# Performance work log

Hardware: AMD Instinct MI355X
Metric: run time of the kernel (lower is better)

The kernel has to match this reference:

```python
import jax, jax.numpy as jnp
import numpy as np

N, E, G = 20000, 320000, 16
IN, HID, OUT, HEADS = 256, 64, 256, 4
D0 = HID * HEADS  # 256, output dim of layer 0 (concat)


def _p(key, shape, scale=0.05):
    return (jax.random.normal(key, shape, dtype=jnp.float32) * scale)


def setup_inputs() -> dict:
    key = jax.random.key(0)
    ks = jax.random.split(key, 24)
    x = jax.random.normal(ks[0], (N, IN), dtype=jnp.float32)
    edge_index = jax.random.randint(ks[1], (2, E), 0, N, dtype=jnp.int64)
    batch = jnp.sort(jax.random.randint(ks[2], (N,), 0, G, dtype=jnp.int64))
    d = {"x": x, "edge_index": edge_index, "batch": batch}
    # Layer 0: TransformerConv(256 -> 64, heads=4, concat=True, beta=True)
    d["Wq0"] = _p(ks[3], (IN, D0)); d["bq0"] = jnp.zeros((D0,), jnp.float32)
    d["Wk0"] = _p(ks[4], (IN, D0)); d["bk0"] = jnp.zeros((D0,), jnp.float32)
    d["Wv0"] = _p(ks[5], (IN, D0)); d["bv0"] = jnp.zeros((D0,), jnp.float32)
    d["Ws0"] = _p(ks[6], (IN, D0)); d["bs0"] = jnp.zeros((D0,), jnp.float32)
    d["Wb0"] = _p(ks[7], (3 * D0, 1))
    d["g0"] = jnp.ones((D0,), jnp.float32); d["b0"] = jnp.zeros((D0,), jnp.float32)
    # Layer 1: TransformerConv(256 -> 256, heads=1, concat=False, beta=True)
    d["Wq1"] = _p(ks[8], (D0, OUT)); d["bq1"] = jnp.zeros((OUT,), jnp.float32)
    d["Wk1"] = _p(ks[9], (D0, OUT)); d["bk1"] = jnp.zeros((OUT,), jnp.float32)
    d["Wv1"] = _p(ks[10], (D0, OUT)); d["bv1"] = jnp.zeros((OUT,), jnp.float32)
    d["Ws1"] = _p(ks[11], (D0, OUT)); d["bs1"] = jnp.zeros((OUT,), jnp.float32)
    d["Wb1"] = _p(ks[12], (3 * OUT, 1))
    d["g1"] = jnp.ones((OUT,), jnp.float32); d["b1"] = jnp.zeros((OUT,), jnp.float32)
    return d


def _transformer_conv(x, src, dst, Wq, bq, Wk, bk, Wv, bv, Ws, bs, Wb, H, C, concat):
    n = x.shape[0]
    q = (x @ Wq + bq).reshape(n, H, C)
    k = (x @ Wk + bk).reshape(n, H, C)
    v = (x @ Wv + bv).reshape(n, H, C)
    # per-edge attention logits [E, H]
    alpha = (q[dst] * k[src]).sum(-1) / jnp.sqrt(jnp.asarray(C, jnp.float32))
    # segment softmax over incoming edges of each dst node
    m = jax.ops.segment_max(alpha, dst, num_segments=n)  # [N, H]
    a = jnp.exp(alpha - m[dst])
    s = jax.ops.segment_sum(a, dst, num_segments=n)  # [N, H]
    a = a / s[dst]
    out = jax.ops.segment_sum(a[:, :, None] * v[src], dst, num_segments=n)  # [N,H,C]
    out = out.reshape(n, H * C) if concat else out.mean(axis=1)
    # beta-gated skip connection
    r = x @ Ws + bs
    g = jax.nn.sigmoid(jnp.concatenate([out, r, out - r], axis=-1) @ Wb)  # [N,1]
    return g * r + (1.0 - g) * out


def _layer_norm(x, g, b, eps=1e-5):
    mu = x.mean(-1, keepdims=True)
    var = x.var(-1, keepdims=True)
    return (x - mu) * jax.lax.rsqrt(var + eps) * g + b


def reference(x, edge_index, batch,
              Wq0, bq0, Wk0, bk0, Wv0, bv0, Ws0, bs0, Wb0, g0, b0,
              Wq1, bq1, Wk1, bk1, Wv1, bv1, Ws1, bs1, Wb1, g1, b1):
    src, dst = edge_index[0], edge_index[1]
    h = _transformer_conv(x, src, dst, Wq0, bq0, Wk0, bk0, Wv0, bv0, Ws0, bs0, Wb0, HEADS, HID, True)
    h = jax.nn.relu(_layer_norm(h, g0, b0))  # dropout is identity at inference
    h = _transformer_conv(h, src, dst, Wq1, bq1, Wk1, bk1, Wv1, bv1, Ws1, bs1, Wb1, 1, OUT, False)
    h = _layer_norm(h, g1, b1)
    # global mean pool over graphs
    sums = jax.ops.segment_sum(h, batch, num_segments=G)
    counts = jax.ops.segment_sum(jnp.ones((h.shape[0],), h.dtype), batch, num_segments=G)
    return sums / jnp.maximum(counts, 1.0)[:, None]
```

## Files before the change

kernel.cpp:

```cpp
#include <hip/hip_runtime.h>
#include <hip/hip_bf16.h>


#define DEVFN static __device__ __forceinline__

typedef __attribute__((ext_vector_type(4))) float f32x4;
typedef __attribute__((ext_vector_type(2))) float f32x2;
typedef __attribute__((ext_vector_type(8))) short bf16x8;

DEVFN float bfu2f(unsigned short u) {
    union { unsigned int i; float f; } t; t.i = ((unsigned)u) << 16; return t.f;
}
DEVFN unsigned short f2bu(float f) {
    __hip_bfloat16 b = __float2bfloat16(f);
    return __builtin_bit_cast(unsigned short, b);
}
DEVFN void stb4(__hip_bfloat16* p, float4 v) {
    ushort4 u;
    u.x = f2bu(v.x); u.y = f2bu(v.y); u.z = f2bu(v.z); u.w = f2bu(v.w);
    *reinterpret_cast<ushort4*>(p) = u;
}
DEVFN float4 f8x4_to_f4(unsigned u) {
    const f32x2 lo = __builtin_amdgcn_cvt_pk_f32_fp8((int)u, false);
    const f32x2 hi = __builtin_amdgcn_cvt_pk_f32_fp8((int)u, true);
    return make_float4(lo.x, lo.y, hi.x, hi.y);
}

DEVFN float dot16(const float* q, uint4 u) {
    const float4 f0 = f8x4_to_f4(u.x);
    const float4 f1 = f8x4_to_f4(u.y);
    const float4 f2 = f8x4_to_f4(u.z);
    const float4 f3 = f8x4_to_f4(u.w);
    float p;
    p = q[0] * f0.x;            p = fmaf(q[1],  f0.y, p);
    p = fmaf(q[2],  f0.z, p);   p = fmaf(q[3],  f0.w, p);
    p = fmaf(q[4],  f1.x, p);   p = fmaf(q[5],  f1.y, p);
    p = fmaf(q[6],  f1.z, p);   p = fmaf(q[7],  f1.w, p);
    p = fmaf(q[8],  f2.x, p);   p = fmaf(q[9],  f2.y, p);
    p = fmaf(q[10], f2.z, p);   p = fmaf(q[11], f2.w, p);
    p = fmaf(q[12], f3.x, p);   p = fmaf(q[13], f3.y, p);
    p = fmaf(q[14], f3.z, p);   p = fmaf(q[15], f3.w, p);
    return p;
}
DEVFN void accum16(float* acc, uint4 u, float a) {
    const float4 f0 = f8x4_to_f4(u.x);
    const float4 f1 = f8x4_to_f4(u.y);
    const float4 f2 = f8x4_to_f4(u.z);
    const float4 f3 = f8x4_to_f4(u.w);
    acc[0]  = fmaf(a, f0.x, acc[0]);  acc[1]  = fmaf(a, f0.y, acc[1]);
    acc[2]  = fmaf(a, f0.z, acc[2]);  acc[3]  = fmaf(a, f0.w, acc[3]);
    acc[4]  = fmaf(a, f1.x, acc[4]);  acc[5]  = fmaf(a, f1.y, acc[5]);
    acc[6]  = fmaf(a, f1.z, acc[6]);  acc[7]  = fmaf(a, f1.w, acc[7]);
    acc[8]  = fmaf(a, f2.x, acc[8]);  acc[9]  = fmaf(a, f2.y, acc[9]);
    acc[10] = fmaf(a, f2.z, acc[10]); acc[11] = fmaf(a, f2.w, acc[11]);
    acc[12] = fmaf(a, f3.x, acc[12]); acc[13] = fmaf(a, f3.y, acc[13]);
    acc[14] = fmaf(a, f3.z, acc[14]); acc[15] = fmaf(a, f3.w, acc[15]);
}

__global__ __launch_bounds__(256)
void wconv_kernel(const float* __restrict__ W0, const float* __restrict__ W1,
                  const float* __restrict__ W2, const float* __restrict__ W3,
                  const float* __restrict__ W4, const float* __restrict__ W5,
                  const float* __restrict__ W6, const float* __restrict__ W7,
                  __hip_bfloat16* __restrict__ Wt)
{
    const float* W;
    switch (blockIdx.y) {
        case 0: W = W0; break; case 1: W = W1; break;
        case 2: W = W2; break; case 3: W = W3; break;
        case 4: W = W4; break; case 5: W = W5; break;
        case 6: W = W6; break; default: W = W7; break;
    }
    const int k = blockIdx.x;
    const int c = threadIdx.x;
    Wt[(size_t)blockIdx.y * 65536 + (size_t)c * 256 + k] =
        __float2bfloat16(W[(size_t)k * 256 + c]);
}

#define SWZ64(r, kb) ((r) * 128 + ((kb) ^ (((r) & 7) << 4)))
#define TSTRIDE 272

template <bool AF32>
__global__ __launch_bounds__(256)
void gemm_mfma_kernel(const void* __restrict__ Av, int M,
                      const __hip_bfloat16* __restrict__ Wt,
                      const float* __restrict__ b0, const float* __restrict__ b1,
                      const float* __restrict__ b2, const float* __restrict__ b3,
                      void* __restrict__ O0, void* __restrict__ O1,
                      void* __restrict__ O2, void* __restrict__ O3,
                      int s0, int s1, int s2, int s3,
                      int f0, int f1, int f2, int f3)
{
    const int q8   = gridDim.x >> 3;
    const int wgid = (blockIdx.x & 7) * q8 + (blockIdx.x >> 3);
    const int rowblk = wgid >> 3;
    const int rem    = wgid & 7;
    const int colblk = rem >> 2;
    const int z      = rem & 3;

    const float* bias; void* O; int rs, isf8;
    switch (z) {
        case 0:  bias = b0; O = O0; rs = s0; isf8 = f0; break;
        case 1:  bias = b1; O = O1; rs = s1; isf8 = f1; break;
        case 2:  bias = b2; O = O2; rs = s2; isf8 = f2; break;
        default: bias = b3; O = O3; rs = s3; isf8 = f3; break;
    }
    const __hip_bfloat16* Wz = Wt + (size_t)z * 65536;

    __shared__ __align__(16) char Sh[128 * TSTRIDE];
    char* As = Sh;
    char* Bs = Sh + 16384;

    const int tid  = threadIdx.x;
    const int row0 = rowblk * 128;
    const int col0 = colblk * 128;
    const int wid  = tid >> 6, lane = tid & 63;
    const int wr   = wid >> 1, wc = wid & 1;
    const int lrow = lane & 15, kg = lane >> 4;

    const int chunk = tid & 7;
    const int rsub  = tid >> 3;

    f32x4 acc[4][4] = {};

    for (int k0 = 0; k0 < 256; k0 += 64) {
        #pragma unroll
        for (int p = 0; p < 4; ++p) {
            const int r  = p * 32 + rsub;
            const int gr = row0 + r;

            if (AF32) {
                const float* Af = (const float*)Av;
                ushort4 lo = {0, 0, 0, 0}, hi = {0, 0, 0, 0};
                if (gr < M) {
                    const float4 a = *reinterpret_cast<const float4*>(
                        Af + (size_t)gr * 256 + k0 + chunk * 8);
                    const float4 b = *reinterpret_cast<const float4*>(
                        Af + (size_t)gr * 256 + k0 + chunk * 8 + 4);
                    lo.x = f2bu(a.x); lo.y = f2bu(a.y); lo.z = f2bu(a.z); lo.w = f2bu(a.w);
                    hi.x = f2bu(b.x); hi.y = f2bu(b.y); hi.z = f2bu(b.z); hi.w = f2bu(b.w);
                }
                *reinterpret_cast<ushort4*>(As + SWZ64(r, chunk * 16))     = lo;
                *reinterpret_cast<ushort4*>(As + SWZ64(r, chunk * 16) + 8) = hi;
            } else {
                const __hip_bfloat16* Ab = (const __hip_bfloat16*)Av;
                ulonglong2 av = {0ull, 0ull};
                if (gr < M)
                    av = *reinterpret_cast<const ulonglong2*>(
                        Ab + (size_t)gr * 256 + k0 + chunk * 8);
                *reinterpret_cast<ulonglong2*>(As + SWZ64(r, chunk * 16)) = av;
            }

            const ulonglong2 bv = *reinterpret_cast<const ulonglong2*>(
                Wz + (size_t)(col0 + r) * 256 + k0 + chunk * 8);
            *reinterpret_cast<ulonglong2*>(Bs + SWZ64(r, chunk * 16)) = bv;
        }
        __syncthreads();

        #pragma unroll
        for (int kk = 0; kk < 64; kk += 32) {
            const int kbyte = kk * 2 + kg * 16;
            bf16x8 af[4], bfr[4];
            #pragma unroll
            for (int m = 0; m < 4; ++m) {
                const int r = wr * 64 + m * 16 + lrow;
                af[m] = *reinterpret_cast<const bf16x8*>(As + SWZ64(r, kbyte));
            }
            #pragma unroll
            for (int n = 0; n < 4; ++n) {
                const int c = wc * 64 + n * 16 + lrow;
                bfr[n] = *reinterpret_cast<const bf16x8*>(Bs + SWZ64(c, kbyte));
            }
            #pragma unroll
            for (int m = 0; m < 4; ++m)
                #pragma unroll
                for (int n = 0; n < 4; ++n)
                    acc[m][n] = __builtin_amdgcn_mfma_f32_16x16x32_bf16(
                        af[m], bfr[n], acc[m][n], 0, 0, 0);
        }
        __syncthreads();
    }

    #pragma unroll
    for (int m = 0; m < 4; ++m) {
        #pragma unroll
        for (int j = 0; j < 4; ++j) {
            const int rr = wr * 64 + m * 16 + kg * 4 + j;
            #pragma unroll
            for (int n = 0; n < 4; ++n) {
                const int cc = wc * 64 + n * 16 + lrow;
                const float v = acc[m][n][j] + bias[col0 + cc];
                *reinterpret_cast<unsigned short*>(Sh + rr * TSTRIDE + cc * 2) = f2bu(v);
            }
        }
    }
    __syncthreads();

    const int row  = tid >> 1;
    const int half = tid & 1;
    const int grow = row0 + row;
    if (grow >= M) return;
    const char* src = Sh + row * TSTRIDE + half * 128;

    if (isf8) {
        unsigned char* dst = (unsigned char*)O + (size_t)grow * rs + col0 + half * 64;
        #pragma unroll
        for (int i2 = 0; i2 < 4; ++i2) {
            uint4 w;
            unsigned tmp[4];
            #pragma unroll
            for (int c8 = 0; c8 < 2; ++c8) {
                const bf16x8 e = *reinterpret_cast<const bf16x8*>(src + (i2 * 2 + c8) * 16);
                const int p0 = __builtin_amdgcn_cvt_pk_fp8_f32(
                    bfu2f((unsigned short)e[0]), bfu2f((unsigned short)e[1]), 0, false);
                const int p1 = __builtin_amdgcn_cvt_pk_fp8_f32(
                    bfu2f((unsigned short)e[2]), bfu2f((unsigned short)e[3]), 0, false);
                const int p2 = __builtin_amdgcn_cvt_pk_fp8_f32(
                    bfu2f((unsigned short)e[4]), bfu2f((unsigned short)e[5]), 0, false);
                const int p3 = __builtin_amdgcn_cvt_pk_fp8_f32(
                    bfu2f((unsigned short)e[6]), bfu2f((unsigned short)e[7]), 0, false);
                tmp[c8 * 2 + 0] = (unsigned)(p0 & 0xFFFF) | ((unsigned)(p1 & 0xFFFF) << 16);
                tmp[c8 * 2 + 1] = (unsigned)(p2 & 0xFFFF) | ((unsigned)(p3 & 0xFFFF) << 16);
            }
            w.x = tmp[0]; w.y = tmp[1]; w.z = tmp[2]; w.w = tmp[3];
            *reinterpret_cast<uint4*>(dst + i2 * 16) = w;
        }
    } else {
        char* dst = (char*)((__hip_bfloat16*)O + (size_t)grow * rs + col0 + half * 64);
        #pragma unroll
        for (int i = 0; i < 8; ++i)
            *reinterpret_cast<ulonglong2*>(dst + i * 16) =
                *reinterpret_cast<const ulonglong2*>(src + i * 16);
    }
}

__global__ __launch_bounds__(256)
void build_kernel(const int* __restrict__ ei, int E, int* __restrict__ deg, int nhist,
                  const int* __restrict__ batch, int N, int* __restrict__ gcount)
{
    if (blockIdx.x < nhist) {
        const int e = blockIdx.x * 256 + threadIdx.x;
        if (e < E) atomicAdd(&deg[ei[E + e]], 1);
    } else {
        __shared__ int h[16];
        if (threadIdx.x < 16) h[threadIdx.x] = 0;
        __syncthreads();
        const int n = (blockIdx.x - nhist) * 256 + threadIdx.x;
        if (n < N) atomicAdd(&h[batch[n]], 1);
        __syncthreads();
        if (threadIdx.x < 16 && h[threadIdx.x] != 0)
            atomicAdd(&gcount[threadIdx.x], h[threadIdx.x]);
    }
}

__global__ __launch_bounds__(1024)
void scan_kernel(const int* __restrict__ deg, int* __restrict__ row_start, int n,
                 const int* __restrict__ gcount, int* __restrict__ gstart)
{
    __shared__ int wsum[16];
    __shared__ int wincl[16];
    const int tid  = threadIdx.x;
    const int w    = tid >> 6;
    const int lane = tid & 63;
    if (tid == 0) {
        row_start[0] = 0;
        int o = 0;
        #pragma unroll
        for (int g = 0; g < 16; ++g) { gstart[g] = o; o += gcount[g]; }
        gstart[16] = o;
    }
    int offset = 0;
    for (int base = 0; base < n; base += 1024) {
        const int idx = base + tid;
        int s = (idx < n) ? deg[idx] : 0;
        #pragma unroll
        for (int d = 1; d < 64; d <<= 1) {
            const int t = __shfl_up(s, d, 64);
            if (lane >= d) s += t;
        }
        if (lane == 63) wsum[w] = s;
        __syncthreads();
        if (tid < 16) {
            int si = wsum[tid];
            #pragma unroll
            for (int d = 1; d < 16; d <<= 1) {
                const int u = __shfl_up(si, d, 64);
                if (tid >= d) si += u;
            }
            wincl[tid] = si;
        }
        __syncthreads();
        const int woff = (w > 0) ? wincl[w - 1] : 0;
        if (idx < n) row_start[idx + 1] = offset + woff + s;
        offset += wincl[15];
        __syncthreads();
    }
}

__global__ __launch_bounds__(256)
void fill_kernel(const int* __restrict__ ei, int E,
                 const int* __restrict__ row_start,
                 int* __restrict__ cursor, int* __restrict__ csr_src)
{
    const int e = blockIdx.x * 256 + threadIdx.x;
    if (e >= E) return;
    const int s = ei[e];
    const int d = ei[E + e];
    const int pos = atomicAdd(&cursor[d], 1);
    csr_src[row_start[d] + pos] = s;
}

template <int NSH, bool RELU, bool OUTB>
__global__ __launch_bounds__(128)
void attn_kernel(const __hip_bfloat16* __restrict__ Q,
                 const unsigned char* __restrict__ KV,
                 const __hip_bfloat16* __restrict__ R,
                 const float* __restrict__ Wb, const float* __restrict__ lng,
                 const float* __restrict__ lnb,
                 const int* __restrict__ row_start, const int* __restrict__ csr_src,
                 __hip_bfloat16* __restrict__ outb, float* __restrict__ outf,
                 int N, float scale)
{
    const int wv   = threadIdx.x >> 6;
    const int lane = threadIdx.x & 63;
    const int g    = lane >> 4;
    const int s    = lane & 15;
    const int node = blockIdx.x * 2 + wv;
    if (node >= N) return;

    float q[16];
    {
        const bf16x8 a = *reinterpret_cast<const bf16x8*>(Q + (size_t)node * 256 + s * 16);
        const bf16x8 b = *reinterpret_cast<const bf16x8*>(Q + (size_t)node * 256 + s * 16 + 8);
        #pragma unroll
        for (int j = 0; j < 8; ++j) {
            q[j]     = bfu2f((unsigned short)a[j]);
            q[8 + j] = bfu2f((unsigned short)b[j]);
        }
    }

    const int beg = row_start[node];
    const int end = row_start[node + 1];

    float acc[16] = {};
    float ssum = 0.f;

    int i = beg + g;
    for (; i + 4 < end; i += 8) {
        const int sa = csr_src[i];
        const int sb = csr_src[i + 4];
        const uint4 ka = *reinterpret_cast<const uint4*>(KV + (size_t)sa * 512 + s * 16);
        const uint4 va = *reinterpret_cast<const uint4*>(KV + (size_t)sa * 512 + 256 + s * 16);
        const uint4 kb = *reinterpret_cast<const uint4*>(KV + (size_t)sb * 512 + s * 16);
        const uint4 vb = *reinterpret_cast<const uint4*>(KV + (size_t)sb * 512 + 256 + s * 16);
        float pa = dot16(q, ka);
        float pb = dot16(q, kb);
        #pragma unroll
        for (int m = 1; m < (1 << NSH); m <<= 1) {
            pa += __shfl_xor(pa, m, 64);
            pb += __shfl_xor(pb, m, 64);
        }
        const float aa = __expf(pa * scale);
        const float ab = __expf(pb * scale);
        ssum += aa + ab;
        accum16(acc, va, aa);
        accum16(acc, vb, ab);
    }
    if (i < end) {
        const int sa = csr_src[i];
        const uint4 ka = *reinterpret_cast<const uint4*>(KV + (size_t)sa * 512 + s * 16);
        const uint4 va = *reinterpret_cast<const uint4*>(KV + (size_t)sa * 512 + 256 + s * 16);
        float pa = dot16(q, ka);
        #pragma unroll
        for (int m = 1; m < (1 << NSH); m <<= 1) pa += __shfl_xor(pa, m, 64);
        const float aa = __expf(pa * scale);
        ssum += aa;
        accum16(acc, va, aa);
    }

    ssum += __shfl_xor(ssum, 16, 64);
    ssum += __shfl_xor(ssum, 32, 64);
    #pragma unroll
    for (int j = 0; j < 16; ++j) {
        acc[j] += __shfl_xor(acc[j], 16, 64);
        acc[j] += __shfl_xor(acc[j], 32, 64);
    }

    if (g != 0) return;

    const float is = (ssum > 0.f) ? 1.f / ssum : 0.f;
    float o[16];
    #pragma unroll
    for (int j = 0; j < 16; ++j) o[j] = acc[j] * is;

    float r[16];
    {
        const bf16x8 a = *reinterpret_cast<const bf16x8*>(R + (size_t)node * 256 + s * 16);
        const bf16x8 b = *reinterpret_cast<const bf16x8*>(R + (size_t)node * 256 + s * 16 + 8);
        #pragma unroll
        for (int j = 0; j < 8; ++j) {
            r[j]     = bfu2f((unsigned short)a[j]);
            r[8 + j] = bfu2f((unsigned short)b[j]);
        }
    }

    float z = 0.f;
    #pragma unroll
    for (int j = 0; j < 16; ++j) {
        const int d = s * 16 + j;
        z += o[j] * Wb[d] + r[j] * Wb[256 + d] + (o[j] - r[j]) * Wb[512 + d];
    }
    #pragma unroll
    for (int m = 1; m < 16; m <<= 1) z += __shfl_xor(z, m, 64);
    const float gg = 1.f / (1.f + __expf(-z));

    float h[16];
    float s1 = 0.f, s2 = 0.f;
    #pragma unroll
    for (int j = 0; j < 16; ++j) {
        h[j] = gg * r[j] + (1.f - gg) * o[j];
        s1 += h[j];
        s2 += h[j] * h[j];
    }
    #pragma unroll
    for (int m = 1; m < 16; m <<= 1) {
        s1 += __shfl_xor(s1, m, 64);
        s2 += __shfl_xor(s2, m, 64);
    }
    const float mu  = s1 * (1.f / 256.f);
    const float var = s2 * (1.f / 256.f) - mu * mu;
    const float inv = rsqrtf(var + 1e-5f);

    #pragma unroll
    for (int j = 0; j < 16; ++j) {
        const int d = s * 16 + j;
        h[j] = (h[j] - mu) * inv * lng[d] + lnb[d];
        if (RELU) h[j] = fmaxf(h[j], 0.f);
    }

    if (OUTB) {
        __hip_bfloat16* dst = outb + (size_t)node * 256 + s * 16;
        stb4(dst,      make_float4(h[0],  h[1],  h[2],  h[3]));
        stb4(dst + 4,  make_float4(h[4],  h[5],  h[6],  h[7]));
        stb4(dst + 8,  make_float4(h[8],  h[9],  h[10], h[11]));
        stb4(dst + 12, make_float4(h[12], h[13], h[14], h[15]));
    } else {
        float* dst = outf + (size_t)node * 256 + s * 16;
        #pragma unroll
        for (int c4 = 0; c4 < 4; ++c4)
            *reinterpret_cast<float4*>(dst + c4 * 4) =
                make_float4(h[c4 * 4], h[c4 * 4 + 1], h[c4 * 4 + 2], h[c4 * 4 + 3]);
    }
}

__global__ __launch_bounds__(256)
void pool_partial_kernel(const float* __restrict__ h, const int* __restrict__ gstart,
                         float* __restrict__ partial)
{
    const int s    = blockIdx.x;
    const int g    = blockIdx.y;
    const int tid  = threadIdx.x;
    const int quad = tid & 63;
    const int sub  = tid >> 6;

    const int beg = gstart[g];
    const int cnt = gstart[g + 1] - beg;

    f32x4 acc = {0.f, 0.f, 0.f, 0.f};
    for (int i = s * 4 + sub; i < cnt; i += 64) {
        const f32x4 v = *reinterpret_cast<const f32x4*>(
            h + (size_t)(beg + i) * 256 + quad * 4);
        acc += v;
    }

    __shared__ f32x4 sh[4][64];
    sh[sub][quad] = acc;
    __syncthreads();
    if (sub == 0) {
        const f32x4 r = sh[0][quad] + sh[1][quad] + sh[2][quad] + sh[3][quad];
        *reinterpret_cast<f32x4*>(partial + ((size_t)(g * 16 + s) * 64 + quad) * 4) = r;
    }
}

__global__ __launch_bounds__(256)
void pool_final_kernel(const float* __restrict__ partial, const int* __restrict__ gcount,
                       float* __restrict__ out)
{
    const int g = blockIdx.x;
    const int d = threadIdx.x;
    float sum = 0.f;
    #pragma unroll
    for (int s = 0; s < 16; ++s)
        sum += partial[(size_t)(g * 16 + s) * 256 + d];
    out[(size_t)g * 256 + d] = sum / (float)max(gcount[g], 1);
}

extern "C" void kernel_launch(void* const* d_in, const int* in_sizes, int n_in,
                              void* d_out, int out_size, void* d_ws, size_t ws_size,
                              hipStream_t stream)
{
    const float* x     = (const float*)d_in[0];
    const int*   ei    = (const int*)d_in[1];
    const int*   batch = (const int*)d_in[2];
    const float* Wq0 = (const float*)d_in[3];  const float* bq0 = (const float*)d_in[4];
    const float* Wk0 = (const float*)d_in[5];  const float* bk0 = (const float*)d_in[6];
    const float* Wv0 = (const float*)d_in[7];  const float* bv0 = (const float*)d_in[8];
    const float* Ws0 = (const float*)d_in[9];  const float* bs0 = (const float*)d_in[10];
    const float* Wb0 = (const float*)d_in[11];
    const float* g0  = (const float*)d_in[12]; const float* b0  = (const float*)d_in[13];
    const float* Wq1 = (const float*)d_in[14]; const float* bq1 = (const float*)d_in[15];
    const float* Wk1 = (const float*)d_in[16]; const float* bk1 = (const float*)d_in[17];
    const float* Wv1 = (const float*)d_in[18]; const float* bv1 = (const float*)d_in[19];
    const float* Ws1 = (const float*)d_in[20]; const float* bs1 = (const float*)d_in[21];
    const float* Wb1 = (const float*)d_in[22];
    const float* g1  = (const float*)d_in[23]; const float* b1  = (const float*)d_in[24];

    const int N = in_sizes[0] / 256;
    const int E = in_sizes[1] / 2;
    const int G = 16;
    const size_t NM = (size_t)N * 256;

    __hip_bfloat16* bws = (__hip_bfloat16*)d_ws;
    __hip_bfloat16* qb  = bws;
    __hip_bfloat16* rb  = qb  + NM;
    __hip_bfloat16* h0b = rb  + NM;
    __hip_bfloat16* wt  = h0b + NM;
    unsigned char* kvb  = (unsigned char*)(wt + 8 * 65536);
    float* h1f     = (float*)(kvb + (size_t)N * 512);
    float* partial = h1f + NM;
    int* deg       = (int*)(partial + 16 * 16 * 256);
    int* row_start = deg + N;
    int* cursor    = row_start + N + 1;
    int* gcount    = cursor + N;
    int* gstart    = gcount + G;
    int* csr_src   = gstart + 17;

    const size_t zbytes = ((size_t)N + (N + 1) + N + G + 17) * sizeof(int);
    hipMemsetAsync(deg, 0, zbytes, stream);

    const int eb = (E + 255) / 256;
    const int nb = (N + 255) / 256;

    wconv_kernel<<<dim3(256, 8), 256, 0, stream>>>(Wq0, Wk0, Wv0, Ws0,
                                                   Wq1, Wk1, Wv1, Ws1, wt);

    build_kernel<<<eb + nb, 256, 0, stream>>>(ei, E, deg, eb, batch, N, gcount);
    scan_kernel<<<1, 1024, 0, stream>>>(deg, row_start, N, gcount, gstart);
    fill_kernel<<<eb, 256, 0, stream>>>(ei, E, row_start, cursor, csr_src);

    const int nrb   = (N + 127) / 128;
    const int ggrid = nrb * 8;
    const int agrid = (N + 1) / 2;

    gemm_mfma_kernel<true><<<ggrid, 256, 0, stream>>>(x, N, wt,
        bq0, bk0, bv0, bs0,
        qb, kvb, kvb + 256, rb,
        256, 512, 512, 256,
        0, 1, 1, 0);
    attn_kernel<2, true, true><<<agrid, 128, 0, stream>>>(
        qb, kvb, rb, Wb0, g0, b0, row_start, csr_src, h0b, nullptr, N, 0.125f);

    gemm_mfma_kernel<false><<<ggrid, 256, 0, stream>>>(h0b, N, wt + 4 * 65536,
        bq1, bk1, bv1, bs1,
        qb, kvb, kvb + 256, rb,
        256, 512, 512, 256,
        0, 1, 1, 0);
    attn_kernel<4, false, false><<<agrid, 128, 0, stream>>>(
        qb, kvb, rb, Wb1, g1, b1, row_start, csr_src, nullptr, h1f, N, 0.0625f);

    pool_partial_kernel<<<dim3(16, 16), 256, 0, stream>>>(h1f, gstart, partial);
    pool_final_kernel<<<16, 256, 0, stream>>>(partial, gcount, (float*)d_out);
}
```

Measured before the change: 232.0 us.

## Pre-convert x to bf16 and stage GEMM tiles with direct global-to-LDS loads

```diff
diff --git a/kernel.cpp b/kernel.cpp
--- a/kernel.cpp
+++ b/kernel.cpp
@@ -7,6 +7,10 @@
 typedef __attribute__((ext_vector_type(4))) float f32x4;
 typedef __attribute__((ext_vector_type(2))) float f32x2;
 typedef __attribute__((ext_vector_type(8))) short bf16x8;
+
+#define GLOAD16(g, lds) __builtin_amdgcn_global_load_lds(                      \
+    (const __attribute__((address_space(1))) unsigned int*)(g),                \
+    (__attribute__((address_space(3))) unsigned int*)(lds), 16, 0, 0)
 
 DEVFN float bfu2f(unsigned short u) {
     union { unsigned int i; float f; } t; t.i = ((unsigned)u) << 16; return t.f;
@@ -58,31 +62,40 @@
 }
 
 __global__ __launch_bounds__(256)
-void wconv_kernel(const float* __restrict__ W0, const float* __restrict__ W1,
-                  const float* __restrict__ W2, const float* __restrict__ W3,
-                  const float* __restrict__ W4, const float* __restrict__ W5,
-                  const float* __restrict__ W6, const float* __restrict__ W7,
-                  __hip_bfloat16* __restrict__ Wt)
-{
-    const float* W;
-    switch (blockIdx.y) {
-        case 0: W = W0; break; case 1: W = W1; break;
-        case 2: W = W2; break; case 3: W = W3; break;
-        case 4: W = W4; break; case 5: W = W5; break;
-        case 6: W = W6; break; default: W = W7; break;
-    }
-    const int k = blockIdx.x;
-    const int c = threadIdx.x;
-    Wt[(size_t)blockIdx.y * 65536 + (size_t)c * 256 + k] =
-        __float2bfloat16(W[(size_t)k * 256 + c]);
+void prep_kernel(const float* __restrict__ x, __hip_bfloat16* __restrict__ xb, int nf2b,
+                 const float* __restrict__ W0, const float* __restrict__ W1,
+                 const float* __restrict__ W2, const float* __restrict__ W3,
+                 const float* __restrict__ W4, const float* __restrict__ W5,
+                 const float* __restrict__ W6, const float* __restrict__ W7,
+                 __hip_bfloat16* __restrict__ Wt)
+{
+    const int b = blockIdx.x;
+    if (b < nf2b) {
+        const int i = b * 256 + threadIdx.x;
+        const float4 v = *reinterpret_cast<const float4*>(x + (size_t)i * 4);
+        stb4(xb + (size_t)i * 4, v);
+    } else {
+        const int wb = b - nf2b;
+        const int z  = wb >> 8;
+        const int k  = wb & 255;
+        const int c  = threadIdx.x;
+        const float* W;
+        switch (z) {
+            case 0: W = W0; break; case 1: W = W1; break;
+            case 2: W = W2; break; case 3: W = W3; break;
+            case 4: W = W4; break; case 5: W = W5; break;
+            case 6: W = W6; break; default: W = W7; break;
+        }
+        Wt[(size_t)z * 65536 + (size_t)c * 256 + k] =
+            __float2bfloat16(W[(size_t)k * 256 + c]);
+    }
 }
 
 #define SWZ64(r, kb) ((r) * 128 + ((kb) ^ (((r) & 7) << 4)))
 #define TSTRIDE 272
 
-template <bool AF32>
 __global__ __launch_bounds__(256)
-void gemm_mfma_kernel(const void* __restrict__ Av, int M,
+void gemm_mfma_kernel(const __hip_bfloat16* __restrict__ A, int M,
                       const __hip_bfloat16* __restrict__ Wt,
                       const float* __restrict__ b0, const float* __restrict__ b1,
                       const float* __restrict__ b2, const float* __restrict__ b3,
@@ -118,42 +131,21 @@
     const int wr   = wid >> 1, wc = wid & 1;
     const int lrow = lane & 15, kg = lane >> 4;
 
-    const int chunk = tid & 7;
-    const int rsub  = tid >> 3;
-
     f32x4 acc[4][4] = {};
 
     for (int k0 = 0; k0 < 256; k0 += 64) {
         #pragma unroll
-        for (int p = 0; p < 4; ++p) {
-            const int r  = p * 32 + rsub;
+        for (int j = 0; j < 4; ++j) {
+            const int s_lin = j * 4096 + wid * 1024 + lane * 16;
+            const int r     = s_lin >> 7;
+            const int kb    = (s_lin & 127) ^ ((r & 7) << 4);
+            const int kelem = k0 + (kb >> 1);
+            char* ldsA = As + j * 4096 + wid * 1024;
+            char* ldsB = Bs + j * 4096 + wid * 1024;
             const int gr = row0 + r;
-
-            if (AF32) {
-                const float* Af = (const float*)Av;
-                ushort4 lo = {0, 0, 0, 0}, hi = {0, 0, 0, 0};
-                if (gr < M) {
-                    const float4 a = *reinterpret_cast<const float4*>(
-                        Af + (size_t)gr * 256 + k0 + chunk * 8);
-                    const float4 b = *reinterpret_cast<const float4*>(
-                        Af + (size_t)gr * 256 + k0 + chunk * 8 + 4);
-                    lo.x = f2bu(a.x); lo.y = f2bu(a.y); lo.z = f2bu(a.z); lo.w = f2bu(a.w);
-                    hi.x = f2bu(b.x); hi.y = f2bu(b.y); hi.z = f2bu(b.z); hi.w = f2bu(b.w);
-                }
-                *reinterpret_cast<ushort4*>(As + SWZ64(r, chunk * 16))     = lo;
-                *reinterpret_cast<ushort4*>(As + SWZ64(r, chunk * 16) + 8) = hi;
-            } else {
-                const __hip_bfloat16* Ab = (const __hip_bfloat16*)Av;
-                ulonglong2 av = {0ull, 0ull};
-                if (gr < M)
-                    av = *reinterpret_cast<const ulonglong2*>(
-                        Ab + (size_t)gr * 256 + k0 + chunk * 8);
-                *reinterpret_cast<ulonglong2*>(As + SWZ64(r, chunk * 16)) = av;
-            }
-
-            const ulonglong2 bv = *reinterpret_cast<const ulonglong2*>(
-                Wz + (size_t)(col0 + r) * 256 + k0 + chunk * 8);
-            *reinterpret_cast<ulonglong2*>(Bs + SWZ64(r, chunk * 16)) = bv;
+            if (gr < M)
+                GLOAD16(A + (size_t)gr * 256 + kelem, ldsA);
+            GLOAD16(Wz + (size_t)(col0 + r) * 256 + kelem, ldsB);
         }
         __syncthreads();
 
@@ -521,7 +513,8 @@
     const size_t NM = (size_t)N * 256;
 
     __hip_bfloat16* bws = (__hip_bfloat16*)d_ws;
-    __hip_bfloat16* qb  = bws;
+    __hip_bfloat16* xb  = bws;
+    __hip_bfloat16* qb  = xb  + NM;
     __hip_bfloat16* rb  = qb  + NM;
     __hip_bfloat16* h0b = rb  + NM;
     __hip_bfloat16* wt  = h0b + NM;
@@ -540,9 +533,10 @@
 
     const int eb = (E + 255) / 256;
     const int nb = (N + 255) / 256;
-
-    wconv_kernel<<<dim3(256, 8), 256, 0, stream>>>(Wq0, Wk0, Wv0, Ws0,
-                                                   Wq1, Wk1, Wv1, Ws1, wt);
+    const int nf2b = (int)((NM / 4 + 255) / 256);
+
+    prep_kernel<<<nf2b + 2048, 256, 0, stream>>>(x, xb, nf2b,
+        Wq0, Wk0, Wv0, Ws0, Wq1, Wk1, Wv1, Ws1, wt);
 
     build_kernel<<<eb + nb, 256, 0, stream>>>(ei, E, deg, eb, batch, N, gcount);
     scan_kernel<<<1, 1024, 0, stream>>>(deg, row_start, N, gcount, gstart);
@@ -552,7 +546,7 @@
     const int ggrid = nrb * 8;
     const int agrid = (N + 1) / 2;
 
-    gemm_mfma_kernel<true><<<ggrid, 256, 0, stream>>>(x, N, wt,
+    gemm_mfma_kernel<<<ggrid, 256, 0, stream>>>(xb, N, wt,
         bq0, bk0, bv0, bs0,
         qb, kvb, kvb + 256, rb,
         256, 512, 512, 256,
@@ -560,7 +554,7 @@
     attn_kernel<2, true, true><<<agrid, 128, 0, stream>>>(
         qb, kvb, rb, Wb0, g0, b0, row_start, csr_src, h0b, nullptr, N, 0.125f);
 
-    gemm_mfma_kernel<false><<<ggrid, 256, 0, stream>>>(h0b, N, wt + 4 * 65536,
+    gemm_mfma_kernel<<<ggrid, 256, 0, stream>>>(h0b, N, wt + 4 * 65536,
         bq1, bk1, bv1, bs1,
         qb, kvb, kvb + 256, rb,
         256, 512, 512, 256,
```

Result: faster. 208.9 us (-10.0%).
